# Kernel optimization log

Measured on AMD Instinct MI355X. Metric: run time of the kernel, lower is better.

Reference implementation:

```python
import jax, jax.numpy as jnp
import numpy as np

N = 40000          # nodes
E = 640000         # edges (avg degree 16)
D_MODEL = 128
H = 8              # num_heads
DH = 16            # d_head
DFF = 512
CLAMP = 5.0
EPS = 1e-5


def setup_inputs() -> dict:
    key = jax.random.key(0)
    ks = jax.random.split(key, 10)
    s = 0.08  # weight init scale
    return {
        "feat": jax.random.normal(ks[0], (N, D_MODEL), dtype=jnp.float32),
        "src": jax.random.randint(ks[1], (E,), 0, N, dtype=jnp.int32),
        "dst": jax.random.randint(ks[2], (E,), 0, N, dtype=jnp.int32),
        "Wq": jax.random.normal(ks[3], (H * DH, D_MODEL), dtype=jnp.float32) * s,
        "Wk": jax.random.normal(ks[4], (H * DH, D_MODEL), dtype=jnp.float32) * s,
        "Wv": jax.random.normal(ks[5], (H * DH, D_MODEL), dtype=jnp.float32) * s,
        "Wo": jax.random.normal(ks[6], (D_MODEL, H * DH), dtype=jnp.float32) * s,
        "ln1_g": jnp.ones((D_MODEL,), jnp.float32),
        "ln1_b": jnp.zeros((D_MODEL,), jnp.float32),
        "W1": jax.random.normal(ks[7], (DFF, D_MODEL), dtype=jnp.float32) * s,
        "b1": jnp.zeros((DFF,), jnp.float32),
        "W2": jax.random.normal(ks[8], (D_MODEL, DFF), dtype=jnp.float32) * s,
        "b2": jnp.zeros((D_MODEL,), jnp.float32),
        "ln2_g": jnp.ones((D_MODEL,), jnp.float32),
        "ln2_b": jnp.zeros((D_MODEL,), jnp.float32),
    }


def _layer_norm(x, g, b):
    mu = jnp.mean(x, axis=-1, keepdims=True)
    var = jnp.mean(jnp.square(x - mu), axis=-1, keepdims=True)
    return (x - mu) * jax.lax.rsqrt(var + EPS) * g + b


def reference(feat, src, dst, Wq, Wk, Wv, Wo, ln1_g, ln1_b, W1, b1, W2, b2, ln2_g, ln2_b):
    n = feat.shape[0]
    # Node-level projections (equivalent to DGL's per-edge Linear on gathered feats)
    q = (feat @ Wq.T).reshape(n, H, DH)
    k = (feat @ Wk.T).reshape(n, H, DH)
    v = (feat @ Wv.T).reshape(n, H, DH)

    # Per-edge multi-head attention logits: q[dst] . k[src] / sqrt(d_head), clamped
    u = jnp.sum(q[dst] * k[src], axis=-1) / np.sqrt(DH)   # [E, H]
    u = jnp.clip(u, -CLAMP, CLAMP)

    # Ragged edge-softmax over incoming edges of each dst node
    m = jax.ops.segment_max(u, dst, num_segments=n)        # [N, H]
    e = jnp.exp(u - m[dst])                                # [E, H]
    denom = jax.ops.segment_sum(e, dst, num_segments=n)    # [N, H]
    a = e / denom[dst]                                     # [E, H]

    # Weighted V scatter-reduce back to dst nodes
    av = (a[:, :, None] * v[src]).reshape(-1, H * DH)      # [E, H*DH]
    sum_av = jax.ops.segment_sum(av, dst, num_segments=n)  # [N, H*DH]
    uh = sum_av @ Wo.T                                     # [N, d_model]

    h1 = _layer_norm(feat + uh, ln1_g, ln1_b)
    ffn = jax.nn.relu(h1 @ W1.T + b1) @ W2.T + b2
    return _layer_norm(h1 + ffn, ln2_g, ln2_b)
```

## Files before the change

### kernel.cpp

```cpp
#include <hip/hip_runtime.h>

#define DM 128
#define DFF 512
#define CLAMP_V 5.0f
#define LN_EPS 1e-5f

typedef __attribute__((ext_vector_type(8))) short bf16x8;
typedef __attribute__((ext_vector_type(4))) float f32x4;

__device__ __forceinline__ float b2f(ushort u) {
  union { uint u; float f; } x; x.u = ((uint)u) << 16; return x.f;
}
__device__ __forceinline__ ushort f2b(float f) {
  union { float f; uint u; } x; x.f = f;
  uint r = x.u + 0x7FFFu + ((x.u >> 16) & 1u);
  return (ushort)(r >> 16);
}
__device__ __forceinline__ void unpackw(uint w, float& lo, float& hi) {
  union { uint u; float f; } A, B;
  A.u = w << 16; B.u = w & 0xFFFF0000u;
  lo = A.f; hi = B.f;
}
__device__ __forceinline__ void unpack8w(uint4 w, float* o) {
  unpackw(w.x, o[0], o[1]); unpackw(w.y, o[2], o[3]);
  unpackw(w.z, o[4], o[5]); unpackw(w.w, o[6], o[7]);
}

__global__ void k_prep(const float* __restrict__ feat,
                       const float* __restrict__ wq, const float* __restrict__ wk,
                       const float* __restrict__ wv, const float* __restrict__ wo,
                       const float* __restrict__ w1, const float* __restrict__ w2,
                       ushort* __restrict__ feat_bf, ushort* __restrict__ wbf,
                       const int* __restrict__ dst, int* __restrict__ deg,
                       int nf4, int castBlocks, int E) {
  if ((int)blockIdx.x >= castBlocks) {
    int e = ((int)blockIdx.x - castBlocks) * 256 + threadIdx.x;
    if (e < E) atomicAdd(&deg[dst[e]], 1);
    return;
  }
  int i = blockIdx.x * 256 + threadIdx.x;
  if (i < nf4) {
    float4 v = *reinterpret_cast<const float4*>(feat + i * 4);
    ushort4 o; o.x = f2b(v.x); o.y = f2b(v.y); o.z = f2b(v.z); o.w = f2b(v.w);
    *reinterpret_cast<ushort4*>(feat_bf + i * 4) = o;
    return;
  }
  int i4 = (i - nf4) * 4;
  if (i4 >= 196608) return;
  const float* s; int o;
  if      (i4 < 16384)  { s = wq; o = i4; }
  else if (i4 < 32768)  { s = wk; o = i4 - 16384; }
  else if (i4 < 49152)  { s = wv; o = i4 - 32768; }
  else if (i4 < 65536)  { s = wo; o = i4 - 49152; }
  else if (i4 < 131072) { s = w1; o = i4 - 65536; }
  else                  { s = w2; o = i4 - 131072; }
  float4 v = *reinterpret_cast<const float4*>(s + o);
  ushort4 u; u.x = f2b(v.x); u.y = f2b(v.y); u.z = f2b(v.z); u.w = f2b(v.w);
  *reinterpret_cast<ushort4*>(wbf + i4) = u;
}

#define SC_EPB 1024

__global__ __launch_bounds__(256) void k_scan1(const int* __restrict__ deg,
                                               int* __restrict__ off,
                                               int* __restrict__ bsum, int n) {
  __shared__ int sh[256];
  const int t = threadIdx.x;
  int base = blockIdx.x * SC_EPB + t * 4;
  int4 v = {0, 0, 0, 0};
  if (base + 3 < n) {
    v = *reinterpret_cast<const int4*>(deg + base);
  } else {
    if (base     < n) v.x = deg[base];
    if (base + 1 < n) v.y = deg[base + 1];
    if (base + 2 < n) v.z = deg[base + 2];
    if (base + 3 < n) v.w = deg[base + 3];
  }
  int s = v.x + v.y + v.z + v.w;
  sh[t] = s;
  __syncthreads();
  #pragma unroll
  for (int d = 1; d < 256; d <<= 1) {
    int x = 0;
    if (t >= d) x = sh[t - d];
    __syncthreads();
    sh[t] += x;
    __syncthreads();
  }
  int ex = sh[t] - s;
  if (base + 3 < n) {
    int4 o; o.x = ex; o.y = ex + v.x; o.z = ex + v.x + v.y; o.w = ex + v.x + v.y + v.z;
    *reinterpret_cast<int4*>(off + base) = o;
  } else {
    if (base     < n) off[base]     = ex;
    if (base + 1 < n) off[base + 1] = ex + v.x;
    if (base + 2 < n) off[base + 2] = ex + v.x + v.y;
    if (base + 3 < n) off[base + 3] = ex + v.x + v.y + v.z;
  }
  if (t == 255) bsum[blockIdx.x] = sh[255];
}

__global__ __launch_bounds__(256) void k_scan3(int* __restrict__ off,
                                               const int* __restrict__ bsum,
                                               int nbk, int n, int E) {
  __shared__ int sadd;
  const int t = threadIdx.x;
  if (t < 64) {
    int v = (t < nbk && t < (int)blockIdx.x) ? bsum[t] : 0;
    #pragma unroll
    for (int msk = 1; msk < 64; msk <<= 1) v += __shfl_xor(v, msk);
    if (t == 0) sadd = v;
  }
  __syncthreads();
  int add = sadd;
  int base = blockIdx.x * SC_EPB + t * 4;
  if (base + 3 < n) {
    int4 v = *reinterpret_cast<int4*>(off + base);
    v.x += add; v.y += add; v.z += add; v.w += add;
    *reinterpret_cast<int4*>(off + base) = v;
  } else {
    if (base     < n) off[base]     += add;
    if (base + 1 < n) off[base + 1] += add;
    if (base + 2 < n) off[base + 2] += add;
  }
  if (blockIdx.x == 0 && t == 0) off[n] = E;
}

__global__ void k_scatter(const int* __restrict__ src, const int* __restrict__ dst,
                          const int* __restrict__ off, int* __restrict__ cur,
                          int* __restrict__ csr, int E) {
  int e = blockIdx.x * blockDim.x + threadIdx.x;
  if (e < E) {
    int d = dst[e];
    int p = off[d] + atomicAdd(&cur[d], 1);
    csr[p] = src[e];
  }
}

template<int FLAGS, bool QKVSPLIT, bool OUTF, bool OUTB>
__global__ __launch_bounds__(512, 2) void k_mmT(
    const ushort* __restrict__ A, const ushort* __restrict__ W,
    const float* __restrict__ bias, const float* __restrict__ res,
    const float* __restrict__ lng, const float* __restrict__ lnbv,
    float* __restrict__ Cf, ushort* __restrict__ Cb, ushort* __restrict__ Cb2,
    int M, int ldc)
{
  __shared__ ushort As[128 * 128];
  __shared__ ushort Bs[128 * 128];
  __shared__ float lnred[(FLAGS & 8) ? 1024 : 4];

  const int tid = threadIdx.x;
  const int wv = tid >> 6, ln = tid & 63;
  const int bnb = blockIdx.x;
  const int mbase = blockIdx.y * 128;
  const int wrow = (wv >> 2) * 64, wcol = (wv & 3) * 32;
  const int o_base = tid * 16;

  #pragma unroll
  for (int is = 0; is < 4; ++is) {
    int o = is * 8192 + o_base;
    int row = o >> 8;
    int c = ((o >> 4) & 15) ^ (row & 15);
    int gr = min(mbase + row, M - 1);
    const ushort* sA = A + (size_t)gr * 128 + c * 8;
    __builtin_amdgcn_global_load_lds(
        (const __attribute__((address_space(1))) void*)sA,
        (__attribute__((address_space(3))) void*)((char*)As + is * 8192 + wv * 1024),
        16, 0, 0);
    const ushort* sB = W + (size_t)(bnb * 128 + row) * 128 + c * 8;
    __builtin_amdgcn_global_load_lds(
        (const __attribute__((address_space(1))) void*)sB,
        (__attribute__((address_space(3))) void*)((char*)Bs + is * 8192 + wv * 1024),
        16, 0, 0);
  }
  __syncthreads();

  f32x4 acc[4][2] = {};
  const char* AsB = (const char*)As;
  const char* BsB = (const char*)Bs;
  #pragma unroll
  for (int kk = 0; kk < 4; ++kk) {
    bf16x8 af[4], bfr[2];
    #pragma unroll
    for (int m = 0; m < 4; ++m) {
      int r = wrow + m * 16 + (ln & 15);
      int c = kk * 4 + (ln >> 4);
      af[m] = *reinterpret_cast<const bf16x8*>(AsB + r * 256 + ((c ^ (r & 15)) << 4));
    }
    #pragma unroll
    for (int n = 0; n < 2; ++n) {
      int r = wcol + n * 16 + (ln & 15);
      int c = kk * 4 + (ln >> 4);
      bfr[n] = *reinterpret_cast<const bf16x8*>(BsB + r * 256 + ((c ^ (r & 15)) << 4));
    }
    #pragma unroll
    for (int m = 0; m < 4; ++m)
      #pragma unroll
      for (int n = 0; n < 2; ++n)
        acc[m][n] = __builtin_amdgcn_mfma_f32_16x16x32_bf16(af[m], bfr[n], acc[m][n], 0, 0, 0);
  }

  if constexpr ((FLAGS & 8) != 0) {
    #pragma unroll
    for (int m = 0; m < 4; ++m)
      #pragma unroll
      for (int n = 0; n < 2; ++n) {
        int gc = wcol + n * 16 + (ln & 15);
        #pragma unroll
        for (int r = 0; r < 4; ++r) {
          int gr = mbase + wrow + m * 16 + (ln >> 4) * 4 + r;
          float v = acc[m][n][r];
          if (FLAGS & 1) v += bias[gc];
          if (FLAGS & 2) v = fmaxf(v, 0.f);
          if (FLAGS & 4) v += res[(size_t)min(gr, M - 1) * 128 + gc];
          acc[m][n][r] = v;
        }
      }
    #pragma unroll
    for (int m = 0; m < 4; ++m)
      #pragma unroll
      for (int r = 0; r < 4; ++r) {
        float sm = acc[m][0][r] + acc[m][1][r];
        float sq = acc[m][0][r] * acc[m][0][r] + acc[m][1][r] * acc[m][1][r];
        #pragma unroll
        for (int msk = 1; msk <= 8; msk <<= 1) {
          sm += __shfl_xor(sm, msk);
          sq += __shfl_xor(sq, msk);
        }
        if ((ln & 15) == 0) {
          int row = wrow + m * 16 + (ln >> 4) * 4 + r;
          lnred[row * 8 + (wv & 3) * 2]     = sm;
          lnred[row * 8 + (wv & 3) * 2 + 1] = sq;
        }
      }
    __syncthreads();
    #pragma unroll
    for (int m = 0; m < 4; ++m)
      #pragma unroll
      for (int r = 0; r < 4; ++r) {
        int row = wrow + m * 16 + (ln >> 4) * 4 + r;
        int gr = mbase + row;
        float sm = lnred[row * 8] + lnred[row * 8 + 2] + lnred[row * 8 + 4] + lnred[row * 8 + 6];
        float sq = lnred[row * 8 + 1] + lnred[row * 8 + 3] + lnred[row * 8 + 5] + lnred[row * 8 + 7];
        float mu = sm * (1.f / 128.f);
        float var = fmaxf(sq * (1.f / 128.f) - mu * mu, 0.f);
        float rstd = rsqrtf(var + LN_EPS);
        if (gr < M) {
          #pragma unroll
          for (int n = 0; n < 2; ++n) {
            int gc = wcol + n * 16 + (ln & 15);
            float y = (acc[m][n][r] - mu) * rstd * lng[gc] + lnbv[gc];
            if (OUTF) Cf[(size_t)gr * 128 + gc] = y;
            if (OUTB) Cb[(size_t)gr * 128 + gc] = f2b(y);
          }
        }
      }
  } else {
    #pragma unroll
    for (int m = 0; m < 4; ++m) {
      int gr0 = mbase + wrow + m * 16 + (ln >> 4) * 4;
      #pragma unroll
      for (int n = 0; n < 2; ++n) {
        int gcl = wcol + n * 16 + (ln & 15);
        float bsv = (FLAGS & 1) ? bias[bnb * 128 + gcl] : 0.f;
        #pragma unroll
        for (int r = 0; r < 4; ++r) {
          int gr = gr0 + r;
          if (gr >= M) continue;
          float v = acc[m][n][r] + bsv;
          if (FLAGS & 2) v = fmaxf(v, 0.f);
          if (QKVSPLIT) {
            if (bnb == 0) Cb[(size_t)gr * 128 + gcl] = f2b(v);
            else          Cb2[(size_t)gr * 256 + (bnb - 1) * 128 + gcl] = f2b(v);
          } else {
            if (OUTF) Cf[(size_t)gr * ldc + bnb * 128 + gcl] = v;
            if (OUTB) Cb[(size_t)gr * ldc + bnb * 128 + gcl] = f2b(v);
          }
        }
      }
    }
  }
}

__global__ __launch_bounds__(512, 2) void k_ffn(
    const ushort* __restrict__ h1b, const float* __restrict__ h1f,
    const ushort* __restrict__ w1, const float* __restrict__ b1,
    const ushort* __restrict__ w2, const float* __restrict__ b2,
    const float* __restrict__ lng, const float* __restrict__ lnbv,
    float* __restrict__ outp, int M)
{
  __shared__ ushort mid[64 * 512];
  __shared__ ushort wbuf[2][128 * 128];

  const int tid = threadIdx.x;
  const int wv = tid >> 6, ln = tid & 63;
  const int lr = ln & 15, hi = ln >> 4;
  const int mbase = blockIdx.x * 64;

  auto STG128 = [&](const ushort* srcBase, int srcLd, int colOff, ushort* dstLds) {
    #pragma unroll
    for (int is = 0; is < 4; ++is) {
      int o = is * 8192 + tid * 16;
      int r = o >> 8;
      int c = ((o >> 4) & 15) ^ (r & 15);
      const ushort* s = srcBase + (size_t)r * srcLd + colOff + c * 8;
      __builtin_amdgcn_global_load_lds(
          (const __attribute__((address_space(1))) void*)s,
          (__attribute__((address_space(3))) void*)((char*)dstLds + is * 8192 + wv * 1024),
          16, 0, 0);
    }
  };

  #pragma unroll
  for (int is = 0; is < 2; ++is) {
    int o = is * 8192 + tid * 16;
    int r = o >> 8;
    int c = ((o >> 4) & 15) ^ (r & 15);
    int gr = min(mbase + r, M - 1);
    const ushort* s = h1b + (size_t)gr * 128 + c * 8;
    __builtin_amdgcn_global_load_lds(
        (const __attribute__((address_space(1))) void*)s,
        (__attribute__((address_space(3))) void*)((char*)mid + is * 8192 + wv * 1024),
        16, 0, 0);
  }
  STG128(w1, 128, 0, wbuf[0]);
  __syncthreads();

  f32x4 p1[4][4] = {};
  const char* hB = (const char*)mid;
  #pragma unroll
  for (int g = 0; g < 4; ++g) {
    const int buf = g & 1;
    if (g < 3) STG128(w1 + (size_t)(g + 1) * 128 * 128, 128, 0, wbuf[buf ^ 1]);
    else       STG128(w2, 512, 0, wbuf[buf ^ 1]);
    const char* wB = (const char*)wbuf[buf];
    #pragma unroll
    for (int kk = 0; kk < 4; ++kk) {
      int c = kk * 4 + hi;
      int wr = wv * 16 + lr;
      bf16x8 aW = *reinterpret_cast<const bf16x8*>(wB + wr * 256 + ((c ^ (wr & 15)) << 4));
      bf16x8 bH[4];
      #pragma unroll
      for (int hj = 0; hj < 4; ++hj) {
        int r = hj * 16 + lr;
        bH[hj] = *reinterpret_cast<const bf16x8*>(hB + r * 256 + ((c ^ (r & 15)) << 4));
      }
      #pragma unroll
      for (int hj = 0; hj < 4; ++hj)
        p1[g][hj] = __builtin_amdgcn_mfma_f32_16x16x32_bf16(aW, bH[hj], p1[g][hj], 0, 0, 0);
    }
    __syncthreads();
  }

  #pragma unroll
  for (int g = 0; g < 4; ++g) {
    int mc0 = g * 128 + wv * 16 + hi * 4;
    float4 bv = *reinterpret_cast<const float4*>(b1 + mc0);
    int chunk = mc0 >> 3;
    int sub = (mc0 & 7) * 2;
    #pragma unroll
    for (int hj = 0; hj < 4; ++hj) {
      int orow = hj * 16 + lr;
      ushort4 pk;
      pk.x = f2b(fmaxf(p1[g][hj][0] + bv.x, 0.f));
      pk.y = f2b(fmaxf(p1[g][hj][1] + bv.y, 0.f));
      pk.z = f2b(fmaxf(p1[g][hj][2] + bv.z, 0.f));
      pk.w = f2b(fmaxf(p1[g][hj][3] + bv.w, 0.f));
      char* dstp = (char*)mid + orow * 1024 + (((chunk & 63) ^ (orow & 15)) << 4) + sub;
      *reinterpret_cast<ushort4*>(dstp) = pk;
    }
  }
  __syncthreads();

  f32x4 p2[4] = {};
  #pragma unroll
  for (int g2 = 0; g2 < 4; ++g2) {
    const int buf = g2 & 1;
    if (g2 < 3) STG128(w2, 512, (g2 + 1) * 128, wbuf[buf ^ 1]);
    const char* wB = (const char*)wbuf[buf];
    #pragma unroll
    for (int kk = 0; kk < 4; ++kk) {
      int wr = wv * 16 + lr;
      int cw = kk * 4 + hi;
      bf16x8 bW = *reinterpret_cast<const bf16x8*>(wB + wr * 256 + ((cw ^ (wr & 15)) << 4));
      int cm = g2 * 16 + kk * 4 + hi;
      bf16x8 aM[4];
      #pragma unroll
      for (int m = 0; m < 4; ++m) {
        int r = m * 16 + lr;
        aM[m] = *reinterpret_cast<const bf16x8*>((const char*)mid + r * 1024 + (((cm & 63) ^ (r & 15)) << 4));
      }
      #pragma unroll
      for (int m = 0; m < 4; ++m)
        p2[m] = __builtin_amdgcn_mfma_f32_16x16x32_bf16(aM[m], bW, p2[m], 0, 0, 0);
    }
    __syncthreads();
  }

  float* lnred = reinterpret_cast<float*>(&wbuf[0][0]);
  {
    int gc = wv * 16 + lr;
    float bsv = b2[gc];
    #pragma unroll
    for (int m = 0; m < 4; ++m)
      #pragma unroll
      for (int r = 0; r < 4; ++r) {
        int gr = mbase + m * 16 + hi * 4 + r;
        p2[m][r] += bsv + h1f[(size_t)min(gr, M - 1) * 128 + gc];
      }
  }
  #pragma unroll
  for (int m = 0; m < 4; ++m)
    #pragma unroll
    for (int r = 0; r < 4; ++r) {
      float sm = p2[m][r];
      float sq = p2[m][r] * p2[m][r];
      #pragma unroll
      for (int msk = 1; msk <= 8; msk <<= 1) {
        sm += __shfl_xor(sm, msk);
        sq += __shfl_xor(sq, msk);
      }
      if (lr == 0) {
        int row = m * 16 + hi * 4 + r;
        lnred[row * 16 + wv * 2]     = sm;
        lnred[row * 16 + wv * 2 + 1] = sq;
      }
    }
  __syncthreads();
  #pragma unroll
  for (int m = 0; m < 4; ++m)
    #pragma unroll
    for (int r = 0; r < 4; ++r) {
      int row = m * 16 + hi * 4 + r;
      int gr = mbase + row;
      float sm = 0.f, sq = 0.f;
      #pragma unroll
      for (int w = 0; w < 8; ++w) {
        sm += lnred[row * 16 + w * 2];
        sq += lnred[row * 16 + w * 2 + 1];
      }
      float mu = sm * (1.f / 128.f);
      float var = fmaxf(sq * (1.f / 128.f) - mu * mu, 0.f);
      float rstd = rsqrtf(var + LN_EPS);
      if (gr < M) {
        int gc = wv * 16 + lr;
        outp[(size_t)gr * 128 + gc] = (p2[m][r] - mu) * rstd * lng[gc] + lnbv[gc];
      }
    }
}

__global__ __launch_bounds__(256) void k_attn(
    const ushort* __restrict__ q, const ushort* __restrict__ kv,
    const int* __restrict__ off, const int* __restrict__ csr,
    ushort* __restrict__ sav, int n)
{
  int node = blockIdx.x * 4 + (threadIdx.x >> 6);
  int lane = threadIdx.x & 63;
  if (node >= n) return;
  const int g = lane >> 3, sl = lane & 7;

  const ushort* qr = q + (size_t)node * 128 + sl * 16;
  uint4 qw0 = *reinterpret_cast<const uint4*>(qr);
  uint4 qw1 = *reinterpret_cast<const uint4*>(qr + 8);
  float qv[16];
  unpack8w(qw0, qv); unpack8w(qw1, qv + 8);

  int b = off[node], e = off[node + 1];
  float s = 0.f;
  float a[16] = {};
  int nIt = (e - b + 7) >> 3;
  int idx = b + g;
  int sn = (b < e) ? csr[min(idx, e - 1)] : 0;

  for (int i = 0; i < nIt; ++i) {
    bool act = idx < e;
    const ushort* kr = kv + (size_t)sn * 256 + sl * 16;
    uint4 kw0 = *reinterpret_cast<const uint4*>(kr);
    uint4 kw1 = *reinterpret_cast<const uint4*>(kr + 8);
    uint4 vw0 = *reinterpret_cast<const uint4*>(kr + 128);
    uint4 vw1 = *reinterpret_cast<const uint4*>(kr + 136);
    idx += 8;
    if (i + 1 < nIt) sn = csr[min(idx, e - 1)];

    float kk[16];
    unpack8w(kw0, kk); unpack8w(kw1, kk + 8);
    float p = 0.f;
    #pragma unroll
    for (int j = 0; j < 16; ++j) p = fmaf(qv[j], kk[j], p);
    float u = fminf(fmaxf(p * 0.25f, -CLAMP_V), CLAMP_V);
    float w = __expf(u - CLAMP_V);
    w = act ? w : 0.f;
    s += w;
    float vvv[16];
    unpack8w(vw0, vvv); unpack8w(vw1, vvv + 8);
    #pragma unroll
    for (int j = 0; j < 16; ++j) a[j] = fmaf(w, vvv[j], a[j]);
  }

  #pragma unroll
  for (int msk = 8; msk <= 32; msk <<= 1) {
    s += __shfl_xor(s, msk);
    #pragma unroll
    for (int j = 0; j < 16; ++j) a[j] += __shfl_xor(a[j], msk);
  }

  float inv = (s > 0.f) ? 1.f / s : 0.f;
  if (g == 0) {
    uint w[8];
    #pragma unroll
    for (int j = 0; j < 8; ++j)
      w[j] = (uint)f2b(a[2 * j] * inv) | ((uint)f2b(a[2 * j + 1] * inv) << 16);
    ushort* outp = sav + (size_t)node * 128 + sl * 16;
    uint4 o0 = {w[0], w[1], w[2], w[3]};
    uint4 o1 = {w[4], w[5], w[6], w[7]};
    *reinterpret_cast<uint4*>(outp) = o0;
    *reinterpret_cast<uint4*>(outp + 8) = o1;
  }
}

extern "C" void kernel_launch(void* const* d_in, const int* in_sizes, int n_in,
                              void* d_out, int out_size, void* d_ws, size_t ws_size,
                              hipStream_t stream)
{
  const float* feat = (const float*)d_in[0];
  const int*   src  = (const int*)d_in[1];
  const int*   dst  = (const int*)d_in[2];
  const float* Wq   = (const float*)d_in[3];
  const float* Wk   = (const float*)d_in[4];
  const float* Wv   = (const float*)d_in[5];
  const float* Wo   = (const float*)d_in[6];
  const float* ln1g = (const float*)d_in[7];
  const float* ln1b = (const float*)d_in[8];
  const float* W1   = (const float*)d_in[9];
  const float* b1   = (const float*)d_in[10];
  const float* W2   = (const float*)d_in[11];
  const float* b2   = (const float*)d_in[12];
  const float* ln2g = (const float*)d_in[13];
  const float* ln2b = (const float*)d_in[14];
  float* out = (float*)d_out;

  const int N = in_sizes[0] / DM;
  const int E = in_sizes[1];
  const size_t NB = (size_t)N;

  char* wsb = (char*)d_ws;
  ushort* q_bf    = (ushort*)wsb;
  ushort* kv_bf   = (ushort*)(wsb + NB * 256);
  ushort* sav_bf  = (ushort*)(wsb + NB * 768);
  float*  h1      = (float*)(wsb + NB * 1024);
  ushort* h1b     = (ushort*)(wsb + NB * 1536);
  ushort* feat_bf = (ushort*)(wsb + NB * 1792);
  ushort* wbf     = (ushort*)(wsb + NB * 2048);
  ushort* wqkv_bf = wbf;
  ushort* wo_bf   = wbf + 49152;
  ushort* w1_bf   = wbf + 65536;
  ushort* w2_bf   = wbf + 131072;
  int* ib  = (int*)(wbf + 196608);
  int* deg = ib;
  int* cur = ib + N;
  int* off = ib + 2 * N;
  int* csr = ib + 3 * N + 1;
  int* bsum = csr + E;

  hipMemsetAsync(deg, 0, 2 * (size_t)N * sizeof(int), stream);

  int nf4 = N * DM / 4;
  int castBlocks = (nf4 + 49152 + 255) / 256;
  int cntBlocks = (E + 255) / 256;
  k_prep<<<castBlocks + cntBlocks, 256, 0, stream>>>(
      feat, Wq, Wk, Wv, Wo, W1, W2, feat_bf, wbf, dst, deg, nf4, castBlocks, E);

  int nbk = (N + SC_EPB - 1) / SC_EPB;
  k_scan1<<<nbk, 256, 0, stream>>>(deg, off, bsum, N);
  k_scan3<<<nbk, 256, 0, stream>>>(off, bsum, nbk, N, E);
  k_scatter<<<cntBlocks, 256, 0, stream>>>(src, dst, off, cur, csr, E);

  int nb4 = (N + 3) / 4;
  const int nT = (N + 127) / 128;

  k_mmT<0, true, false, true><<<dim3(3, nT), 512, 0, stream>>>(
      feat_bf, wqkv_bf, nullptr, nullptr, nullptr, nullptr,
      nullptr, q_bf, kv_bf, N, 128);

  k_attn<<<nb4, 256, 0, stream>>>(q_bf, kv_bf, off, csr, sav_bf, N);

  k_mmT<4 | 8, false, true, true><<<dim3(1, nT), 512, 0, stream>>>(
      sav_bf, wo_bf, nullptr, feat, ln1g, ln1b, h1, h1b, nullptr, N, 128);

  const int nF = (N + 63) / 64;
  k_ffn<<<nF, 512, 0, stream>>>(
      h1b, h1, w1_bf, b1, w2_bf, b2, ln2g, ln2b, out, N);
}
```

Baseline: 193.2 us.

## Fuse Wo projection and LayerNorm1 into FFN kernel; merge scan kernels

Moves the output projection, residual add and first LayerNorm into the FFN kernel, so h1 stays in registers and LDS instead of being written to global memory and read back in fp32 and bf16. The LDS buffers are repurposed to stage weights for Wo, W1 and W2. The two-pass scan is replaced by a single kernel in which each block re-sums the preceding degrees itself and also zeroes the cursor array, which shrinks the memset and removes one launch. The cost is redundant prefix reads in the scan and a more complex, register-heavier fused kernel.

```diff
diff --git a/kernel.cpp b/kernel.cpp
--- a/kernel.cpp
+++ b/kernel.cpp
@@ -61,12 +61,28 @@
 
 #define SC_EPB 1024
 
-__global__ __launch_bounds__(256) void k_scan1(const int* __restrict__ deg,
-                                               int* __restrict__ off,
-                                               int* __restrict__ bsum, int n) {
+__global__ __launch_bounds__(256) void k_scan(const int* __restrict__ deg,
+                                              int* __restrict__ off,
+                                              int* __restrict__ cur,
+                                              int n, int E) {
   __shared__ int sh[256];
+  __shared__ int wsum[4];
   const int t = threadIdx.x;
-  int base = blockIdx.x * SC_EPB + t * 4;
+  const int bstart = blockIdx.x * SC_EPB;
+
+  int gs = 0;
+  for (int base = t * 4; base < bstart; base += SC_EPB) {
+    int4 v = *reinterpret_cast<const int4*>(deg + base);
+    gs += v.x + v.y + v.z + v.w;
+  }
+  #pragma unroll
+  for (int m = 1; m < 64; m <<= 1) gs += __shfl_xor(gs, m);
+  if ((t & 63) == 0) wsum[t >> 6] = gs;
+  __syncthreads();
+  int gadd = wsum[0] + wsum[1] + wsum[2] + wsum[3];
+  __syncthreads();
+
+  int base = bstart + t * 4;
   int4 v = {0, 0, 0, 0};
   if (base + 3 < n) {
     v = *reinterpret_cast<const int4*>(deg + base);
@@ -87,41 +103,17 @@
     sh[t] += x;
     __syncthreads();
   }
-  int ex = sh[t] - s;
+  int ex = sh[t] - s + gadd;
   if (base + 3 < n) {
     int4 o; o.x = ex; o.y = ex + v.x; o.z = ex + v.x + v.y; o.w = ex + v.x + v.y + v.z;
     *reinterpret_cast<int4*>(off + base) = o;
+    int4 z = {0, 0, 0, 0};
+    *reinterpret_cast<int4*>(cur + base) = z;
   } else {
-    if (base     < n) off[base]     = ex;
-    if (base + 1 < n) off[base + 1] = ex + v.x;
-    if (base + 2 < n) off[base + 2] = ex + v.x + v.y;
-    if (base + 3 < n) off[base + 3] = ex + v.x + v.y + v.z;
-  }
-  if (t == 255) bsum[blockIdx.x] = sh[255];
-}
-
-__global__ __launch_bounds__(256) void k_scan3(int* __restrict__ off,
-                                               const int* __restrict__ bsum,
-                                               int nbk, int n, int E) {
-  __shared__ int sadd;
-  const int t = threadIdx.x;
-  if (t < 64) {
-    int v = (t < nbk && t < (int)blockIdx.x) ? bsum[t] : 0;
-    #pragma unroll
-    for (int msk = 1; msk < 64; msk <<= 1) v += __shfl_xor(v, msk);
-    if (t == 0) sadd = v;
-  }
-  __syncthreads();
-  int add = sadd;
-  int base = blockIdx.x * SC_EPB + t * 4;
-  if (base + 3 < n) {
-    int4 v = *reinterpret_cast<int4*>(off + base);
-    v.x += add; v.y += add; v.z += add; v.w += add;
-    *reinterpret_cast<int4*>(off + base) = v;
-  } else {
-    if (base     < n) off[base]     += add;
-    if (base + 1 < n) off[base + 1] += add;
-    if (base + 2 < n) off[base + 2] += add;
+    if (base     < n) { off[base]     = ex;                    cur[base]     = 0; }
+    if (base + 1 < n) { off[base + 1] = ex + v.x;              cur[base + 1] = 0; }
+    if (base + 2 < n) { off[base + 2] = ex + v.x + v.y;        cur[base + 2] = 0; }
+    if (base + 3 < n) { off[base + 3] = ex + v.x + v.y + v.z;  cur[base + 3] = 0; }
   }
   if (blockIdx.x == 0 && t == 0) off[n] = E;
 }
@@ -137,17 +129,13 @@
   }
 }
 
-template<int FLAGS, bool QKVSPLIT, bool OUTF, bool OUTB>
+template<int FLAGS>
 __global__ __launch_bounds__(512, 2) void k_mmT(
     const ushort* __restrict__ A, const ushort* __restrict__ W,
-    const float* __restrict__ bias, const float* __restrict__ res,
-    const float* __restrict__ lng, const float* __restrict__ lnbv,
-    float* __restrict__ Cf, ushort* __restrict__ Cb, ushort* __restrict__ Cb2,
-    int M, int ldc)
+    ushort* __restrict__ Cb, ushort* __restrict__ Cb2, int M)
 {
   __shared__ ushort As[128 * 128];
   __shared__ ushort Bs[128 * 128];
-  __shared__ float lnred[(FLAGS & 8) ? 1024 : 4];
 
   const int tid = threadIdx.x;
   const int wv = tid >> 6, ln = tid & 63;
@@ -200,93 +188,31 @@
         acc[m][n] = __builtin_amdgcn_mfma_f32_16x16x32_bf16(af[m], bfr[n], acc[m][n], 0, 0, 0);
   }
 
-  if constexpr ((FLAGS & 8) != 0) {
-    #pragma unroll
-    for (int m = 0; m < 4; ++m)
-      #pragma unroll
-      for (int n = 0; n < 2; ++n) {
-        int gc = wcol + n * 16 + (ln & 15);
-        #pragma unroll
-        for (int r = 0; r < 4; ++r) {
-          int gr = mbase + wrow + m * 16 + (ln >> 4) * 4 + r;
-          float v = acc[m][n][r];
-          if (FLAGS & 1) v += bias[gc];
-          if (FLAGS & 2) v = fmaxf(v, 0.f);
-          if (FLAGS & 4) v += res[(size_t)min(gr, M - 1) * 128 + gc];
-          acc[m][n][r] = v;
-        }
-      }
-    #pragma unroll
-    for (int m = 0; m < 4; ++m)
+  #pragma unroll
+  for (int m = 0; m < 4; ++m) {
+    int gr0 = mbase + wrow + m * 16 + (ln >> 4) * 4;
+    #pragma unroll
+    for (int n = 0; n < 2; ++n) {
+      int gcl = wcol + n * 16 + (ln & 15);
       #pragma unroll
       for (int r = 0; r < 4; ++r) {
-        float sm = acc[m][0][r] + acc[m][1][r];
-        float sq = acc[m][0][r] * acc[m][0][r] + acc[m][1][r] * acc[m][1][r];
-        #pragma unroll
-        for (int msk = 1; msk <= 8; msk <<= 1) {
-          sm += __shfl_xor(sm, msk);
-          sq += __shfl_xor(sq, msk);
-        }
-        if ((ln & 15) == 0) {
-          int row = wrow + m * 16 + (ln >> 4) * 4 + r;
-          lnred[row * 8 + (wv & 3) * 2]     = sm;
-          lnred[row * 8 + (wv & 3) * 2 + 1] = sq;
-        }
-      }
-    __syncthreads();
-    #pragma unroll
-    for (int m = 0; m < 4; ++m)
-      #pragma unroll
-      for (int r = 0; r < 4; ++r) {
-        int row = wrow + m * 16 + (ln >> 4) * 4 + r;
-        int gr = mbase + row;
-        float sm = lnred[row * 8] + lnred[row * 8 + 2] + lnred[row * 8 + 4] + lnred[row * 8 + 6];
-        float sq = lnred[row * 8 + 1] + lnred[row * 8 + 3] + lnred[row * 8 + 5] + lnred[row * 8 + 7];
-        float mu = sm * (1.f / 128.f);
-        float var = fmaxf(sq * (1.f / 128.f) - mu * mu, 0.f);
-        float rstd = rsqrtf(var + LN_EPS);
-        if (gr < M) {
-          #pragma unroll
-          for (int n = 0; n < 2; ++n) {
-            int gc = wcol + n * 16 + (ln & 15);
-            float y = (acc[m][n][r] - mu) * rstd * lng[gc] + lnbv[gc];
-            if (OUTF) Cf[(size_t)gr * 128 + gc] = y;
-            if (OUTB) Cb[(size_t)gr * 128 + gc] = f2b(y);
-          }
-        }
-      }
-  } else {
-    #pragma unroll
-    for (int m = 0; m < 4; ++m) {
-      int gr0 = mbase + wrow + m * 16 + (ln >> 4) * 4;
-      #pragma unroll
-      for (int n = 0; n < 2; ++n) {
-        int gcl = wcol + n * 16 + (ln & 15);
-        float bsv = (FLAGS & 1) ? bias[bnb * 128 + gcl] : 0.f;
-        #pragma unroll
-        for (int r = 0; r < 4; ++r) {
-          int gr = gr0 + r;
-          if (gr >= M) continue;
-          float v = acc[m][n][r] + bsv;
-          if (FLAGS & 2) v = fmaxf(v, 0.f);
-          if (QKVSPLIT) {
-            if (bnb == 0) Cb[(size_t)gr * 128 + gcl] = f2b(v);
-            else          Cb2[(size_t)gr * 256 + (bnb - 1) * 128 + gcl] = f2b(v);
-          } else {
-            if (OUTF) Cf[(size_t)gr * ldc + bnb * 128 + gcl] = v;
-            if (OUTB) Cb[(size_t)gr * ldc + bnb * 128 + gcl] = f2b(v);
-          }
-        }
-      }
-    }
-  }
-}
-
-__global__ __launch_bounds__(512, 2) void k_ffn(
-    const ushort* __restrict__ h1b, const float* __restrict__ h1f,
+        int gr = gr0 + r;
+        if (gr >= M) continue;
+        float v = acc[m][n][r];
+        if (bnb == 0) Cb[(size_t)gr * 128 + gcl] = f2b(v);
+        else          Cb2[(size_t)gr * 256 + (bnb - 1) * 128 + gcl] = f2b(v);
+      }
+    }
+  }
+}
+
+__global__ __launch_bounds__(512, 2) void k_fused(
+    const ushort* __restrict__ sav, const float* __restrict__ feat,
+    const ushort* __restrict__ wo,
+    const float* __restrict__ ln1g, const float* __restrict__ ln1b,
     const ushort* __restrict__ w1, const float* __restrict__ b1,
     const ushort* __restrict__ w2, const float* __restrict__ b2,
-    const float* __restrict__ lng, const float* __restrict__ lnbv,
+    const float* __restrict__ ln2g, const float* __restrict__ ln2b,
     float* __restrict__ outp, int M)
 {
   __shared__ ushort mid[64 * 512];
@@ -296,8 +222,11 @@
   const int wv = tid >> 6, ln = tid & 63;
   const int lr = ln & 15, hi = ln >> 4;
   const int mbase = blockIdx.x * 64;
-
-  auto STG128 = [&](const ushort* srcBase, int srcLd, int colOff, ushort* dstLds) {
+  char* M0 = (char*)mid;
+  char* M1 = (char*)mid + 16384;
+  char* M2 = (char*)mid + 32768;
+
+  auto STG128 = [&](const ushort* srcBase, int srcLd, int colOff, char* dstLds) {
     #pragma unroll
     for (int is = 0; is < 4; ++is) {
       int o = is * 8192 + tid * 16;
@@ -306,7 +235,7 @@
       const ushort* s = srcBase + (size_t)r * srcLd + colOff + c * 8;
       __builtin_amdgcn_global_load_lds(
           (const __attribute__((address_space(1))) void*)s,
-          (__attribute__((address_space(3))) void*)((char*)dstLds + is * 8192 + wv * 1024),
+          (__attribute__((address_space(3))) void*)(dstLds + is * 8192 + wv * 1024),
           16, 0, 0);
     }
   };
@@ -317,23 +246,100 @@
     int r = o >> 8;
     int c = ((o >> 4) & 15) ^ (r & 15);
     int gr = min(mbase + r, M - 1);
-    const ushort* s = h1b + (size_t)gr * 128 + c * 8;
+    const ushort* s = sav + (size_t)gr * 128 + c * 8;
     __builtin_amdgcn_global_load_lds(
         (const __attribute__((address_space(1))) void*)s,
-        (__attribute__((address_space(3))) void*)((char*)mid + is * 8192 + wv * 1024),
+        (__attribute__((address_space(3))) void*)(M1 + is * 8192 + wv * 1024),
         16, 0, 0);
   }
-  STG128(w1, 128, 0, wbuf[0]);
+  STG128(wo, 128, 0, (char*)wbuf[0]);
+  STG128(w1, 128, 0, M2);
+  __syncthreads();
+
+  const int gc = wv * 16 + lr;
+
+  f32x4 p0[4] = {};
+  {
+    const char* wB = (const char*)wbuf[0];
+    #pragma unroll
+    for (int kk = 0; kk < 4; ++kk) {
+      int c = kk * 4 + hi;
+      int wr = wv * 16 + lr;
+      bf16x8 bWo = *reinterpret_cast<const bf16x8*>(wB + wr * 256 + ((c ^ (wr & 15)) << 4));
+      bf16x8 aS[4];
+      #pragma unroll
+      for (int m = 0; m < 4; ++m) {
+        int r = m * 16 + lr;
+        aS[m] = *reinterpret_cast<const bf16x8*>(M1 + r * 256 + ((c ^ (r & 15)) << 4));
+      }
+      #pragma unroll
+      for (int m = 0; m < 4; ++m)
+        p0[m] = __builtin_amdgcn_mfma_f32_16x16x32_bf16(aS[m], bWo, p0[m], 0, 0, 0);
+    }
+  }
+  #pragma unroll
+  for (int m = 0; m < 4; ++m)
+    #pragma unroll
+    for (int r = 0; r < 4; ++r) {
+      int gr = mbase + m * 16 + hi * 4 + r;
+      p0[m][r] += feat[(size_t)min(gr, M - 1) * 128 + gc];
+    }
+  float* lnred = reinterpret_cast<float*>(&wbuf[1][0]);
+  #pragma unroll
+  for (int m = 0; m < 4; ++m)
+    #pragma unroll
+    for (int r = 0; r < 4; ++r) {
+      float sm = p0[m][r];
+      float sq = p0[m][r] * p0[m][r];
+      #pragma unroll
+      for (int msk = 1; msk <= 8; msk <<= 1) {
+        sm += __shfl_xor(sm, msk);
+        sq += __shfl_xor(sq, msk);
+      }
+      if (lr == 0) {
+        int row = m * 16 + hi * 4 + r;
+        lnred[row * 16 + wv * 2]     = sm;
+        lnred[row * 16 + wv * 2 + 1] = sq;
+      }
+    }
+  __syncthreads();
+  STG128(w1 + 16384, 128, 0, (char*)wbuf[0]);
+  {
+    float g1v = ln1g[gc], bb1 = ln1b[gc];
+    int chunk = gc >> 3;
+    int sub = (gc & 7) * 2;
+    #pragma unroll
+    for (int m = 0; m < 4; ++m)
+      #pragma unroll
+      for (int r = 0; r < 4; ++r) {
+        int row = m * 16 + hi * 4 + r;
+        float sm = 0.f, sq = 0.f;
+        #pragma unroll
+        for (int w = 0; w < 8; ++w) {
+          sm += lnred[row * 16 + w * 2];
+          sq += lnred[row * 16 + w * 2 + 1];
+        }
+        float mu = sm * (1.f / 128.f);
+        float var = fmaxf(sq * (1.f / 128.f) - mu * mu, 0.f);
+        float rstd = rsqrtf(var + LN_EPS);
+        float y = (p0[m][r] - mu) * rstd * g1v + bb1;
+        p0[m][r] = y;
+        *reinterpret_cast<ushort*>(M0 + row * 256 + ((chunk ^ (row & 15)) << 4) + sub) = f2b(y);
+      }
+  }
   __syncthreads();
 
   f32x4 p1[4][4] = {};
-  const char* hB = (const char*)mid;
   #pragma unroll
   for (int g = 0; g < 4; ++g) {
-    const int buf = g & 1;
-    if (g < 3) STG128(w1 + (size_t)(g + 1) * 128 * 128, 128, 0, wbuf[buf ^ 1]);
-    else       STG128(w2, 512, 0, wbuf[buf ^ 1]);
-    const char* wB = (const char*)wbuf[buf];
+    if (g == 0) STG128(w1 + 2 * 16384, 128, 0, (char*)wbuf[1]);
+    if (g == 1) STG128(w1 + 3 * 16384, 128, 0, M2);
+    if (g == 2) STG128(w2, 512, 0,   (char*)wbuf[0]);
+    if (g == 3) STG128(w2, 512, 128, (char*)wbuf[1]);
+    const char* wB = (g == 0) ? M2
+                   : (g == 1) ? (const char*)wbuf[0]
+                   : (g == 2) ? (const char*)wbuf[1]
+                   : M2;
     #pragma unroll
     for (int kk = 0; kk < 4; ++kk) {
       int c = kk * 4 + hi;
@@ -343,7 +349,7 @@
       #pragma unroll
       for (int hj = 0; hj < 4; ++hj) {
         int r = hj * 16 + lr;
-        bH[hj] = *reinterpret_cast<const bf16x8*>(hB + r * 256 + ((c ^ (r & 15)) << 4));
+        bH[hj] = *reinterpret_cast<const bf16x8*>(M0 + r * 256 + ((c ^ (r & 15)) << 4));
       }
       #pragma unroll
       for (int hj = 0; hj < 4; ++hj)
@@ -375,9 +381,9 @@
   f32x4 p2[4] = {};
   #pragma unroll
   for (int g2 = 0; g2 < 4; ++g2) {
-    const int buf = g2 & 1;
-    if (g2 < 3) STG128(w2, 512, (g2 + 1) * 128, wbuf[buf ^ 1]);
-    const char* wB = (const char*)wbuf[buf];
+    if (g2 == 1) STG128(w2, 512, 256, (char*)wbuf[0]);
+    if (g2 == 2) STG128(w2, 512, 384, (char*)wbuf[1]);
+    const char* wB = (const char*)wbuf[g2 & 1];
     #pragma unroll
     for (int kk = 0; kk < 4; ++kk) {
       int wr = wv * 16 + lr;
@@ -397,17 +403,14 @@
     __syncthreads();
   }
 
-  float* lnred = reinterpret_cast<float*>(&wbuf[0][0]);
+  lnred = reinterpret_cast<float*>(&wbuf[0][0]);
   {
-    int gc = wv * 16 + lr;
     float bsv = b2[gc];
     #pragma unroll
     for (int m = 0; m < 4; ++m)
       #pragma unroll
-      for (int r = 0; r < 4; ++r) {
-        int gr = mbase + m * 16 + hi * 4 + r;
-        p2[m][r] += bsv + h1f[(size_t)min(gr, M - 1) * 128 + gc];
-      }
+      for (int r = 0; r < 4; ++r)
+        p2[m][r] += bsv + p0[m][r];
   }
   #pragma unroll
   for (int m = 0; m < 4; ++m)
@@ -427,26 +430,27 @@
       }
     }
   __syncthreads();
-  #pragma unroll
-  for (int m = 0; m < 4; ++m)
-    #pragma unroll
-    for (int r = 0; r < 4; ++r) {
-      int row = m * 16 + hi * 4 + r;
-      int gr = mbase + row;
-      float sm = 0.f, sq = 0.f;
-      #pragma unroll
-      for (int w = 0; w < 8; ++w) {
-        sm += lnred[row * 16 + w * 2];
-        sq += lnred[row * 16 + w * 2 + 1];
-      }
-      float mu = sm * (1.f / 128.f);
-      float var = fmaxf(sq * (1.f / 128.f) - mu * mu, 0.f);
-      float rstd = rsqrtf(var + LN_EPS);
-      if (gr < M) {
-        int gc = wv * 16 + lr;
-        outp[(size_t)gr * 128 + gc] = (p2[m][r] - mu) * rstd * lng[gc] + lnbv[gc];
-      }
-    }
+  {
+    float g2v = ln2g[gc], bb2 = ln2b[gc];
+    #pragma unroll
+    for (int m = 0; m < 4; ++m)
+      #pragma unroll
+      for (int r = 0; r < 4; ++r) {
+        int row = m * 16 + hi * 4 + r;
+        int gr = mbase + row;
+        float sm = 0.f, sq = 0.f;
+        #pragma unroll
+        for (int w = 0; w < 8; ++w) {
+          sm += lnred[row * 16 + w * 2];
+          sq += lnred[row * 16 + w * 2 + 1];
+        }
+        float mu = sm * (1.f / 128.f);
+        float var = fmaxf(sq * (1.f / 128.f) - mu * mu, 0.f);
+        float rstd = rsqrtf(var + LN_EPS);
+        if (gr < M)
+          outp[(size_t)gr * 128 + gc] = (p2[m][r] - mu) * rstd * g2v + bb2;
+      }
+  }
 }
 
 __global__ __launch_bounds__(256) void k_attn(
@@ -547,8 +551,6 @@
   ushort* q_bf    = (ushort*)wsb;
   ushort* kv_bf   = (ushort*)(wsb + NB * 256);
   ushort* sav_bf  = (ushort*)(wsb + NB * 768);
-  float*  h1      = (float*)(wsb + NB * 1024);
-  ushort* h1b     = (ushort*)(wsb + NB * 1536);
   ushort* feat_bf = (ushort*)(wsb + NB * 1792);
   ushort* wbf     = (ushort*)(wsb + NB * 2048);
   ushort* wqkv_bf = wbf;
@@ -560,9 +562,8 @@
   int* cur = ib + N;
   int* off = ib + 2 * N;
   int* csr = ib + 3 * N + 1;
-  int* bsum = csr + E;
-
-  hipMemsetAsync(deg, 0, 2 * (size_t)N * sizeof(int), stream);
+
+  hipMemsetAsync(deg, 0, (size_t)N * sizeof(int), stream);
 
   int nf4 = N * DM / 4;
   int castBlocks = (nf4 + 49152 + 255) / 256;
@@ -571,23 +572,17 @@
       feat, Wq, Wk, Wv, Wo, W1, W2, feat_bf, wbf, dst, deg, nf4, castBlocks, E);
 
   int nbk = (N + SC_EPB - 1) / SC_EPB;
-  k_scan1<<<nbk, 256, 0, stream>>>(deg, off, bsum, N);
-  k_scan3<<<nbk, 256, 0, stream>>>(off, bsum, nbk, N, E);
+  k_scan<<<nbk, 256, 0, stream>>>(deg, off, cur, N, E);
   k_scatter<<<cntBlocks, 256, 0, stream>>>(src, dst, off, cur, csr, E);
 
   int nb4 = (N + 3) / 4;
   const int nT = (N + 127) / 128;
 
-  k_mmT<0, true, false, true><<<dim3(3, nT), 512, 0, stream>>>(
-      feat_bf, wqkv_bf, nullptr, nullptr, nullptr, nullptr,
-      nullptr, q_bf, kv_bf, N, 128);
+  k_mmT<0><<<dim3(3, nT), 512, 0, stream>>>(feat_bf, wqkv_bf, q_bf, kv_bf, N);
 
   k_attn<<<nb4, 256, 0, stream>>>(q_bf, kv_bf, off, csr, sav_bf, N);
 
-  k_mmT<4 | 8, false, true, true><<<dim3(1, nT), 512, 0, stream>>>(
-      sav_bf, wo_bf, nullptr, feat, ln1g, ln1b, h1, h1b, nullptr, N, 128);
-
   const int nF = (N + 63) / 64;
-  k_ffn<<<nF, 512, 0, stream>>>(
-      h1b, h1, w1_bf, b1, w2_bf, b2, ln2g, ln2b, out, N);
-}
+  k_fused<<<nF, 512, 0, stream>>>(
+      sav_bf, feat, wo_bf, ln1g, ln1b, w1_bf, b1, w2_bf, b2, ln2g, ln2b, out, N);
+}
```

Measured after the change: 196.8 us. No clear change (+1.9%).
